# Optimization experiments

Measured on AMD Instinct MI355X. Metric: run time of the kernel, lower is better.

## Reference

```python
import jax, jax.numpy as jnp
import numpy as np

N = 4096
IN_DIM = 512
NUM_HEADS = 8
SUB_DIM = 64
ETA = 0.5
LAMBDA_SPARSE = 0.1
EDGE_PROB = 0.01


def setup_inputs() -> dict:
    key = jax.random.key(0)
    k_h, k_u, k_a = jax.random.split(key, 3)
    H = jax.random.normal(k_h, (N, IN_DIM), dtype=jnp.float32)
    # Per-head orthonormal subspace bases (QR init, as in the torch module)
    raw = jax.random.normal(k_u, (NUM_HEADS, IN_DIM, SUB_DIM), dtype=jnp.float32)
    U = jax.vmap(lambda a: jnp.linalg.qr(a)[0])(raw)  # [K, in_dim, r]
    # Binary adjacency mask with self-loops (float 0/1)
    adj = (jax.random.uniform(k_a, (N, N)) < EDGE_PROB).astype(jnp.float32)
    adj_mask = jnp.maximum(adj, jnp.eye(N, dtype=jnp.float32))
    threshold = jnp.full((IN_DIM,), LAMBDA_SPARSE, dtype=jnp.float32)
    return {"H": H, "adj_mask": adj_mask, "U": U, "threshold": threshold}


def reference(H, adj_mask, U, threshold):
    r = U.shape[-1]
    scale = jnp.asarray(r, H.dtype) ** 0.5
    # Z_k = U_k^T H^T  -> [K, r, n]
    Z = jnp.einsum('kdr,nd->krn', U, H)
    # scores[k, i, j] = Z_k[:, i] . Z_k[:, j] / sqrt(r), masked to neighbors
    scores = jnp.einsum('kri,krj->kij', Z, Z) / scale
    scores = scores + (1.0 - adj_mask) * (-1e9)
    alpha = jax.nn.softmax(scores, axis=-1)          # [K, n, n]
    # Z_agg[k, :, i] = sum_j alpha[k, i, j] * Z_k[:, j]
    Z_agg = jnp.einsum('krj,kij->kri', Z, alpha)      # [K, r, n]
    # project back and sum heads: [n, d]
    agg = jnp.einsum('kdr,kri->id', U, Z_agg)
    H_half = H + ETA * agg
    H_out = jax.nn.relu(H_half - threshold[None, :])
    # orthogonality loss: sum_{k<l} ||U_k^T U_l||_F^2
    gram = jnp.einsum('kdr,lds->klrs', U, U)
    sq = jnp.sum(gram ** 2, axis=(-1, -2))            # [K, K]
    orth_loss = 0.5 * (jnp.sum(sq) - jnp.trace(sq))
    return H_out, orth_loss
```

## Files before the change

### kernel.cpp

```cpp
#include <hip/hip_runtime.h>
#include <hip/hip_bf16.h>

#define NN   4096
#define DD   512
#define KH   8
#define RR   64
#define CAP  128

typedef unsigned short u16;
typedef unsigned int   u32;
typedef __attribute__((ext_vector_type(8))) short short8;
typedef __attribute__((ext_vector_type(4))) float f32x4;

__device__ __forceinline__ float bflo(u32 v){ union{u32 i; float f;} c; c.i = v << 16;        return c.f; }
__device__ __forceinline__ float bfhi(u32 v){ union{u32 i; float f;} c; c.i = v & 0xFFFF0000u; return c.f; }
__device__ __forceinline__ u16 f2bf(float f){ __hip_bfloat16 h = __float2bfloat16(f); return *reinterpret_cast<u16*>(&h); }

__global__ __launch_bounds__(256) void prep_all(const float* __restrict__ H, const float* __restrict__ U,
                                                u16* __restrict__ Hb, u16* __restrict__ Bt1,
                                                u16* __restrict__ Bt2, float* __restrict__ lossA,
                                                int* __restrict__ doneA) {
    __shared__ float tile[64][65];
    int b = blockIdx.x, t = threadIdx.x;
    if (b < 2048) {
        size_t id = (size_t)b * 256 + t;
        float4 v = *(const float4*)(H + id * 4);
        ushort4 o; o.x = f2bf(v.x); o.y = f2bf(v.y); o.z = f2bf(v.z); o.w = f2bf(v.w);
        *(ushort4*)(Hb + id * 4) = o;
        return;
    }
    if (b == 2112) { if (t == 0) { lossA[0] = 0.f; doneA[0] = 0; } return; }
    int b2 = b - 2048;
    int k = b2 >> 3, d0 = (b2 & 7) * 64;
    #pragma unroll
    for (int s = 0; s < 4; s++) {
        int u = t + 256 * s;
        int dd = u >> 4, rq = u & 15;
        float4 v = *(const float4*)(U + ((size_t)(k * DD + d0 + dd)) * RR + rq * 4);
        tile[dd][rq * 4 + 0] = v.x; tile[dd][rq * 4 + 1] = v.y;
        tile[dd][rq * 4 + 2] = v.z; tile[dd][rq * 4 + 3] = v.w;
    }
    __syncthreads();
    {
        int r = t >> 2;
        #pragma unroll
        for (int ii = 0; ii < 16; ii++) {
            int dd = (t & 3) * 16 + ii;
            Bt1[(size_t)(k * RR + r) * DD + d0 + dd] = f2bf(tile[dd][r]);
        }
    }
    {
        int dd = t >> 2, rb = (t & 3) * 16;
        #pragma unroll
        for (int ii = 0; ii < 16; ii++) {
            Bt2[(size_t)(d0 + dd) * DD + k * RR + rb + ii] = f2bf(tile[dd][rb + ii]);
        }
    }
}

__global__ __launch_bounds__(256) void zgemm_mfma(const u16* __restrict__ Hb, const u16* __restrict__ Bt1,
                                                  u16* __restrict__ Zb) {
    __shared__ short As[64][72];
    __shared__ short Bs[64][72];
    const int t = threadIdx.x;
    const int i0 = blockIdx.x * 64, n0 = blockIdx.y * 64;
    const int w = t >> 6, lane = t & 63;
    const int lm = lane & 15, lg = lane >> 4;
    f32x4 acc[4] = {};
    for (int kc = 0; kc < DD; kc += 64) {
        #pragma unroll
        for (int s = 0; s < 2; s++) {
            int c = t + 256 * s; int row = c >> 3, g = c & 7;
            *(short8*)&As[row][g * 8] = *(const short8*)(Hb  + (size_t)(i0 + row) * DD + kc + g * 8);
            *(short8*)&Bs[row][g * 8] = *(const short8*)(Bt1 + (size_t)(n0 + row) * DD + kc + g * 8);
        }
        __syncthreads();
        #pragma unroll
        for (int ks = 0; ks < 64; ks += 32) {
            short8 af = *(const short8*)&As[w * 16 + lm][ks + lg * 8];
            #pragma unroll
            for (int b = 0; b < 4; b++) {
                short8 bfr = *(const short8*)&Bs[b * 16 + lm][ks + lg * 8];
                acc[b] = __builtin_amdgcn_mfma_f32_16x16x32_bf16(af, bfr, acc[b], 0, 0, 0);
            }
        }
        __syncthreads();
    }
    #pragma unroll
    for (int b = 0; b < 4; b++)
        #pragma unroll
        for (int q = 0; q < 4; q++) {
            int row = i0 + w * 16 + lg * 4 + q;
            int col = n0 + b * 16 + lm;
            Zb[(size_t)row * DD + col] = f2bf(acc[b][q]);
        }
}

__global__ __launch_bounds__(512) void attn5(const u16* __restrict__ Zb, const float* __restrict__ adj,
                                             u16* __restrict__ Zaggb) {
    const int i = blockIdx.x, t = threadIdx.x;
    const int k = t >> 6, lane = t & 63;
    __shared__ int   nbrS[CAP + 32];
    __shared__ int   cntS;
    __shared__ float ziS[DD];
    __shared__ short zbuf[KH][32][72];
    if (t == 0) cntS = 0;
    __syncthreads();
    const float* arow = adj + (size_t)i * NN;
    #pragma unroll
    for (int qq = 0; qq < 2; qq++) {
        int j = (qq * 512 + t) * 4;
        float4 mv = *(const float4*)(arow + j);
        if (mv.x != 0.f) { int p = atomicAdd(&cntS, 1); if (p < CAP) nbrS[p] = j;     }
        if (mv.y != 0.f) { int p = atomicAdd(&cntS, 1); if (p < CAP) nbrS[p] = j + 1; }
        if (mv.z != 0.f) { int p = atomicAdd(&cntS, 1); if (p < CAP) nbrS[p] = j + 2; }
        if (mv.w != 0.f) { int p = atomicAdd(&cntS, 1); if (p < CAP) nbrS[p] = j + 3; }
    }
    if (t < 256) {
        u32 v = *(const u32*)(Zb + (size_t)i * DD + t * 2);
        ziS[t * 2] = bflo(v); ziS[t * 2 + 1] = bfhi(v);
    }
    __syncthreads();
    const int ci = min(cntS, CAP);
    if (t < 32) nbrS[ci + t] = nbrS[0];
    __syncthreads();

    const int n = lane >> 1, h = lane & 1;
    const int half = lane >> 5, L = lane & 31;
    const float4* zi4 = (const float4*)(ziS + k * 64 + h * 32);
    float m = -3.0e38f, l = 0.f, accA = 0.f, accB = 0.f;

    for (int base = 0; base < ci; base += 32) {
        const int cact = min(32, ci - base);
        const int j = nbrS[base + n];
        const uint4* zp = (const uint4*)(Zb + (size_t)j * DD + k * 64 + h * 32);
        uint4 v0 = zp[0], v1 = zp[1], v2 = zp[2], v3 = zp[3];
        *(uint4*)&zbuf[k][n][h * 32 + 0]  = v0;
        *(uint4*)&zbuf[k][n][h * 32 + 8]  = v1;
        *(uint4*)&zbuf[k][n][h * 32 + 16] = v2;
        *(uint4*)&zbuf[k][n][h * 32 + 24] = v3;
        float4 a0 = zi4[0], a1 = zi4[1], a2 = zi4[2], a3 = zi4[3];
        float4 a4 = zi4[4], a5 = zi4[5], a6 = zi4[6], a7 = zi4[7];
        float s = bflo(v0.x)*a0.x + bfhi(v0.x)*a0.y + bflo(v0.y)*a0.z + bfhi(v0.y)*a0.w
                + bflo(v0.z)*a1.x + bfhi(v0.z)*a1.y + bflo(v0.w)*a1.z + bfhi(v0.w)*a1.w
                + bflo(v1.x)*a2.x + bfhi(v1.x)*a2.y + bflo(v1.y)*a2.z + bfhi(v1.y)*a2.w
                + bflo(v1.z)*a3.x + bfhi(v1.z)*a3.y + bflo(v1.w)*a3.z + bfhi(v1.w)*a3.w
                + bflo(v2.x)*a4.x + bfhi(v2.x)*a4.y + bflo(v2.y)*a4.z + bfhi(v2.y)*a4.w
                + bflo(v2.z)*a5.x + bfhi(v2.z)*a5.y + bflo(v2.w)*a5.z + bfhi(v2.w)*a5.w
                + bflo(v3.x)*a6.x + bfhi(v3.x)*a6.y + bflo(v3.y)*a6.z + bfhi(v3.y)*a6.w
                + bflo(v3.z)*a7.x + bfhi(v3.z)*a7.y + bflo(v3.w)*a7.z + bfhi(v3.w)*a7.w;
        s += __shfl_xor(s, 1);
        s *= 0.125f;
        if (n >= cact) s = -3.0e38f;
        float mx = s;
        #pragma unroll
        for (int off = 2; off < 64; off <<= 1) mx = fmaxf(mx, __shfl_xor(mx, off));
        const float mnew = fmaxf(m, mx);
        const float scale = __expf(m - mnew);
        const float e = (n < cact) ? __expf(s - mnew) : 0.f;
        float se = h ? 0.f : e;
        #pragma unroll
        for (int off = 1; off < 64; off <<= 1) se += __shfl_xor(se, off);
        l = l * scale + se;
        m = mnew;
        accA *= scale; accB *= scale;
        for (int c = half; c < cact; c += 2) {
            const float wgt = __shfl(e, 2 * c);
            u32 z2 = *(const u32*)&zbuf[k][c][2 * L];
            accA += wgt * bflo(z2);
            accB += wgt * bfhi(z2);
        }
    }
    accA += __shfl_xor(accA, 32);
    accB += __shfl_xor(accB, 32);
    if (lane < 32) {
        const float inv = 1.0f / l;
        u32 o = ((u32)f2bf(accA * inv)) | (((u32)f2bf(accB * inv)) << 16);
        *(u32*)(Zaggb + (size_t)i * DD + k * 64 + 2 * L) = o;
    }
}

__global__ __launch_bounds__(256) void outgemm_mfma(const u16* __restrict__ Ab, const u16* __restrict__ Btb,
                                                    const float* __restrict__ H, const float* __restrict__ thr,
                                                    float* __restrict__ out) {
    __shared__ short As[64][72];
    __shared__ short Bs[64][72];
    const int t = threadIdx.x;
    const int i0 = blockIdx.x * 64, n0 = blockIdx.y * 64;
    const int w = t >> 6, lane = t & 63;
    const int lm = lane & 15, lg = lane >> 4;
    f32x4 acc[4] = {};
    for (int kc = 0; kc < DD; kc += 64) {
        #pragma unroll
        for (int s = 0; s < 2; s++) {
            int c = t + 256 * s; int row = c >> 3, g = c & 7;
            *(short8*)&As[row][g * 8] = *(const short8*)(Ab  + (size_t)(i0 + row) * DD + kc + g * 8);
            *(short8*)&Bs[row][g * 8] = *(const short8*)(Btb + (size_t)(n0 + row) * DD + kc + g * 8);
        }
        __syncthreads();
        #pragma unroll
        for (int ks = 0; ks < 64; ks += 32) {
            short8 af = *(const short8*)&As[w * 16 + lm][ks + lg * 8];
            #pragma unroll
            for (int b = 0; b < 4; b++) {
                short8 bfr = *(const short8*)&Bs[b * 16 + lm][ks + lg * 8];
                acc[b] = __builtin_amdgcn_mfma_f32_16x16x32_bf16(af, bfr, acc[b], 0, 0, 0);
            }
        }
        __syncthreads();
    }
    #pragma unroll
    for (int b = 0; b < 4; b++) {
        const int col = n0 + b * 16 + lm;
        const float th = thr[col];
        #pragma unroll
        for (int q = 0; q < 4; q++) {
            int row = i0 + w * 16 + lg * 4 + q;
            float h = H[(size_t)row * DD + col];
            out[(size_t)row * DD + col] = fmaxf(h + 0.5f * acc[b][q] - th, 0.f);
        }
    }
}

__global__ __launch_bounds__(256) void orth_kernel(const float* __restrict__ U, float* __restrict__ loss,
                                                   int* __restrict__ done, float* __restrict__ outLoss) {
    __shared__ float UkT[64][20];
    __shared__ float UlT[64][68];
    const int pb = blockIdx.x >> 2, strip = blockIdx.x & 3;
    int idx = pb, k = 0, lh = 1;
    #pragma unroll
    for (int kk = 0; kk < 8; kk++) {
        int c = 7 - kk;
        if (idx < c) { k = kk; lh = kk + 1 + idx; break; }
        idx -= c;
    }
    const int t = threadIdx.x;
    const int r = t & 15;
    const int s0 = (t >> 4) * 4;
    const int r0g = strip * 16;
    const float* Uk = U + (size_t)k  * DD * RR;
    const float* Ul = U + (size_t)lh * DD * RR;
    float a0 = 0.f, a1 = 0.f, a2 = 0.f, a3 = 0.f;
    for (int dc = 0; dc < DD; dc += 64) {
        {   int dd = t >> 2, rq = t & 3;
            *(float4*)&UkT[dd][rq * 4] = *(const float4*)(Uk + (size_t)(dc + dd) * RR + r0g + rq * 4);
        }
        #pragma unroll
        for (int s = 0; s < 4; s++) {
            int u = t + 256 * s;
            int dd = u >> 4, sq = u & 15;
            *(float4*)&UlT[dd][sq * 4] = *(const float4*)(Ul + (size_t)(dc + dd) * RR + sq * 4);
        }
        __syncthreads();
        #pragma unroll 4
        for (int dd = 0; dd < 64; dd++) {
            float a = UkT[dd][r];
            float4 b = *(const float4*)&UlT[dd][s0];
            a0 += a * b.x; a1 += a * b.y; a2 += a * b.z; a3 += a * b.w;
        }
        __syncthreads();
    }
    float v = a0 * a0 + a1 * a1 + a2 * a2 + a3 * a3;
    #pragma unroll
    for (int off = 32; off; off >>= 1) v += __shfl_down(v, off, 64);
    __shared__ float red[4];
    if ((t & 63) == 0) red[t >> 6] = v;
    __syncthreads();
    if (t == 0) {
        atomicAdd(loss, red[0] + red[1] + red[2] + red[3]);
        __threadfence();
        int d = atomicAdd(done, 1);
        if (d == 111) {
            float total = atomicAdd(loss, 0.f);
            outLoss[0] = total;
        }
    }
}

extern "C" void kernel_launch(void* const* d_in, const int* in_sizes, int n_in,
                              void* d_out, int out_size, void* d_ws, size_t ws_size,
                              hipStream_t stream) {
    const float* H   = (const float*)d_in[0];
    const float* adj = (const float*)d_in[1];
    const float* U   = (const float*)d_in[2];
    const float* thr = (const float*)d_in[3];
    float* out = (float*)d_out;

    char* ws = (char*)d_ws;
    float* lossA = (float*)ws;
    int*   doneA = (int*)(ws + 64);
    u16*   Hb    = (u16*)(ws + 1024);
    u16*   Zb    = (u16*)(ws + 1024 + 4u * 1024 * 1024);
    u16*   Zaggb = (u16*)(ws + 1024 + 8u * 1024 * 1024);
    u16*   Bt1   = (u16*)(ws + 1024 + 12u * 1024 * 1024);
    u16*   Bt2   = (u16*)(ws + 1024 + 12u * 1024 * 1024 + 512u * 1024);

    prep_all<<<2113, 256, 0, stream>>>(H, U, Hb, Bt1, Bt2, lossA, doneA);
    zgemm_mfma<<<dim3(64, 8), 256, 0, stream>>>(Hb, Bt1, Zb);
    attn5<<<NN, 512, 0, stream>>>(Zb, adj, Zaggb);
    outgemm_mfma<<<dim3(64, 8), 256, 0, stream>>>(Zaggb, Bt2, H, thr, out);
    orth_kernel<<<112, 256, 0, stream>>>(U, lossA, doneA, out + (size_t)NN * DD);
}
```

Before: 179.6 us.

## Fuse adjacency scan, Z GEMM and orth loss into one kernel; slim attention tiles

Result: slower. 197.5 us (+10.0%).

```diff
diff --git a/kernel.cpp b/kernel.cpp
--- a/kernel.cpp
+++ b/kernel.cpp
@@ -58,115 +58,177 @@
     }
 }
 
-__global__ __launch_bounds__(256) void zgemm_mfma(const u16* __restrict__ Hb, const u16* __restrict__ Bt1,
-                                                  u16* __restrict__ Zb) {
-    __shared__ short As[64][72];
-    __shared__ short Bs[64][72];
-    const int t = threadIdx.x;
-    const int i0 = blockIdx.x * 64, n0 = blockIdx.y * 64;
-    const int w = t >> 6, lane = t & 63;
-    const int lm = lane & 15, lg = lane >> 4;
-    f32x4 acc[4] = {};
-    for (int kc = 0; kc < DD; kc += 64) {
-        #pragma unroll
-        for (int s = 0; s < 2; s++) {
-            int c = t + 256 * s; int row = c >> 3, g = c & 7;
-            *(short8*)&As[row][g * 8] = *(const short8*)(Hb  + (size_t)(i0 + row) * DD + kc + g * 8);
-            *(short8*)&Bs[row][g * 8] = *(const short8*)(Bt1 + (size_t)(n0 + row) * DD + kc + g * 8);
-        }
-        __syncthreads();
-        #pragma unroll
-        for (int ks = 0; ks < 64; ks += 32) {
-            short8 af = *(const short8*)&As[w * 16 + lm][ks + lg * 8];
+struct GemmSh { short As[64][72]; short Bs[64][72]; };
+struct OrthSh { float UkT[64][20]; float UlT[64][68]; float red[4]; };
+struct ScanSh { int cnt; };
+union  MidSh  { GemmSh g; OrthSh o; ScanSh s; };
+
+__global__ __launch_bounds__(256) void mid_kernel(const u16* __restrict__ Hb, const u16* __restrict__ Bt1,
+                                                  u16* __restrict__ Zb,
+                                                  const float* __restrict__ adj, int* __restrict__ nlist,
+                                                  int* __restrict__ cnt,
+                                                  const float* __restrict__ U, float* __restrict__ loss,
+                                                  int* __restrict__ done, float* __restrict__ outLoss) {
+    __shared__ MidSh sh;
+    const int b = blockIdx.x, t = threadIdx.x;
+    if (b < 4096) {
+        const int i = b;
+        if (t == 0) sh.s.cnt = 0;
+        __syncthreads();
+        const float* arow = adj + (size_t)i * NN;
+        #pragma unroll
+        for (int qq = 0; qq < 4; qq++) {
+            int j = (qq * 256 + t) * 4;
+            float4 mv = *(const float4*)(arow + j);
+            if (mv.x != 0.f) { int p = atomicAdd(&sh.s.cnt, 1); if (p < CAP) nlist[(size_t)i * CAP + p] = j;     }
+            if (mv.y != 0.f) { int p = atomicAdd(&sh.s.cnt, 1); if (p < CAP) nlist[(size_t)i * CAP + p] = j + 1; }
+            if (mv.z != 0.f) { int p = atomicAdd(&sh.s.cnt, 1); if (p < CAP) nlist[(size_t)i * CAP + p] = j + 2; }
+            if (mv.w != 0.f) { int p = atomicAdd(&sh.s.cnt, 1); if (p < CAP) nlist[(size_t)i * CAP + p] = j + 3; }
+        }
+        __syncthreads();
+        if (t == 0) cnt[i] = min(sh.s.cnt, CAP);
+        return;
+    }
+    if (b < 4608) {
+        const int bb = b - 4096;
+        const int i0 = (bb & 63) * 64, n0 = (bb >> 6) * 64;
+        const int w = t >> 6, lane = t & 63;
+        const int lm = lane & 15, lg = lane >> 4;
+        f32x4 acc[4] = {};
+        for (int kc = 0; kc < DD; kc += 64) {
             #pragma unroll
-            for (int b = 0; b < 4; b++) {
-                short8 bfr = *(const short8*)&Bs[b * 16 + lm][ks + lg * 8];
-                acc[b] = __builtin_amdgcn_mfma_f32_16x16x32_bf16(af, bfr, acc[b], 0, 0, 0);
+            for (int s = 0; s < 2; s++) {
+                int c = t + 256 * s; int row = c >> 3, g = c & 7;
+                *(short8*)&sh.g.As[row][g * 8] = *(const short8*)(Hb  + (size_t)(i0 + row) * DD + kc + g * 8);
+                *(short8*)&sh.g.Bs[row][g * 8] = *(const short8*)(Bt1 + (size_t)(n0 + row) * DD + kc + g * 8);
             }
-        }
-        __syncthreads();
-    }
+            __syncthreads();
+            #pragma unroll
+            for (int ks = 0; ks < 64; ks += 32) {
+                short8 af = *(const short8*)&sh.g.As[w * 16 + lm][ks + lg * 8];
+                #pragma unroll
+                for (int bq = 0; bq < 4; bq++) {
+                    short8 bfr = *(const short8*)&sh.g.Bs[bq * 16 + lm][ks + lg * 8];
+                    acc[bq] = __builtin_amdgcn_mfma_f32_16x16x32_bf16(af, bfr, acc[bq], 0, 0, 0);
+                }
+            }
+            __syncthreads();
+        }
+        #pragma unroll
+        for (int bq = 0; bq < 4; bq++)
+            #pragma unroll
+            for (int q = 0; q < 4; q++) {
+                int row = i0 + w * 16 + lg * 4 + q;
+                int col = n0 + bq * 16 + lm;
+                Zb[(size_t)row * DD + col] = f2bf(acc[bq][q]);
+            }
+        return;
+    }
+    const int ob = b - 4608;
+    const int pb = ob >> 2, strip = ob & 3;
+    int idx = pb, k = 0, lh = 1;
     #pragma unroll
-    for (int b = 0; b < 4; b++)
-        #pragma unroll
-        for (int q = 0; q < 4; q++) {
-            int row = i0 + w * 16 + lg * 4 + q;
-            int col = n0 + b * 16 + lm;
-            Zb[(size_t)row * DD + col] = f2bf(acc[b][q]);
-        }
-}
-
-__global__ __launch_bounds__(512) void attn5(const u16* __restrict__ Zb, const float* __restrict__ adj,
-                                             u16* __restrict__ Zaggb) {
+    for (int kk = 0; kk < 8; kk++) {
+        int c = 7 - kk;
+        if (idx < c) { k = kk; lh = kk + 1 + idx; break; }
+        idx -= c;
+    }
+    const int r = t & 15;
+    const int s0 = (t >> 4) * 4;
+    const int r0g = strip * 16;
+    const float* Uk = U + (size_t)k  * DD * RR;
+    const float* Ul = U + (size_t)lh * DD * RR;
+    float a0 = 0.f, a1 = 0.f, a2 = 0.f, a3 = 0.f;
+    for (int dc = 0; dc < DD; dc += 64) {
+        {   int dd = t >> 2, rq = t & 3;
+            *(float4*)&sh.o.UkT[dd][rq * 4] = *(const float4*)(Uk + (size_t)(dc + dd) * RR + r0g + rq * 4);
+        }
+        #pragma unroll
+        for (int s = 0; s < 4; s++) {
+            int u = t + 256 * s;
+            int dd = u >> 4, sq = u & 15;
+            *(float4*)&sh.o.UlT[dd][sq * 4] = *(const float4*)(Ul + (size_t)(dc + dd) * RR + sq * 4);
+        }
+        __syncthreads();
+        #pragma unroll 4
+        for (int dd = 0; dd < 64; dd++) {
+            float a = sh.o.UkT[dd][r];
+            float4 bv = *(const float4*)&sh.o.UlT[dd][s0];
+            a0 += a * bv.x; a1 += a * bv.y; a2 += a * bv.z; a3 += a * bv.w;
+        }
+        __syncthreads();
+    }
+    float v = a0 * a0 + a1 * a1 + a2 * a2 + a3 * a3;
+    #pragma unroll
+    for (int off = 32; off; off >>= 1) v += __shfl_down(v, off, 64);
+    if ((t & 63) == 0) sh.o.red[t >> 6] = v;
+    __syncthreads();
+    if (t == 0) {
+        atomicAdd(loss, sh.o.red[0] + sh.o.red[1] + sh.o.red[2] + sh.o.red[3]);
+        __threadfence();
+        int d = atomicAdd(done, 1);
+        if (d == 111) {
+            float total = atomicAdd(loss, 0.f);
+            outLoss[0] = total;
+        }
+    }
+}
+
+__global__ __launch_bounds__(512) void attn6(const u16* __restrict__ Zb, const int* __restrict__ nlist,
+                                             const int* __restrict__ cnt, u16* __restrict__ Zaggb) {
     const int i = blockIdx.x, t = threadIdx.x;
     const int k = t >> 6, lane = t & 63;
-    __shared__ int   nbrS[CAP + 32];
-    __shared__ int   cntS;
+    __shared__ int   nbrS[CAP + 16];
     __shared__ float ziS[DD];
-    __shared__ short zbuf[KH][32][72];
-    if (t == 0) cntS = 0;
-    __syncthreads();
-    const float* arow = adj + (size_t)i * NN;
-    #pragma unroll
-    for (int qq = 0; qq < 2; qq++) {
-        int j = (qq * 512 + t) * 4;
-        float4 mv = *(const float4*)(arow + j);
-        if (mv.x != 0.f) { int p = atomicAdd(&cntS, 1); if (p < CAP) nbrS[p] = j;     }
-        if (mv.y != 0.f) { int p = atomicAdd(&cntS, 1); if (p < CAP) nbrS[p] = j + 1; }
-        if (mv.z != 0.f) { int p = atomicAdd(&cntS, 1); if (p < CAP) nbrS[p] = j + 2; }
-        if (mv.w != 0.f) { int p = atomicAdd(&cntS, 1); if (p < CAP) nbrS[p] = j + 3; }
-    }
+    __shared__ u32   zbufU[KH][16][36];
+    const int ci = cnt[i];
+    for (int u = t; u < ci; u += 512) nbrS[u] = nlist[(size_t)i * CAP + u];
     if (t < 256) {
         u32 v = *(const u32*)(Zb + (size_t)i * DD + t * 2);
         ziS[t * 2] = bflo(v); ziS[t * 2 + 1] = bfhi(v);
     }
     __syncthreads();
-    const int ci = min(cntS, CAP);
-    if (t < 32) nbrS[ci + t] = nbrS[0];
+    if (t < 16) nbrS[ci + t] = nbrS[0];
     __syncthreads();
 
-    const int n = lane >> 1, h = lane & 1;
+    const int n = lane >> 2, q = lane & 3;
     const int half = lane >> 5, L = lane & 31;
-    const float4* zi4 = (const float4*)(ziS + k * 64 + h * 32);
+    const float4* zi4 = (const float4*)(ziS + k * 64 + q * 16);
     float m = -3.0e38f, l = 0.f, accA = 0.f, accB = 0.f;
 
-    for (int base = 0; base < ci; base += 32) {
-        const int cact = min(32, ci - base);
+    for (int base = 0; base < ci; base += 16) {
+        const int cact = min(16, ci - base);
         const int j = nbrS[base + n];
-        const uint4* zp = (const uint4*)(Zb + (size_t)j * DD + k * 64 + h * 32);
-        uint4 v0 = zp[0], v1 = zp[1], v2 = zp[2], v3 = zp[3];
-        *(uint4*)&zbuf[k][n][h * 32 + 0]  = v0;
-        *(uint4*)&zbuf[k][n][h * 32 + 8]  = v1;
-        *(uint4*)&zbuf[k][n][h * 32 + 16] = v2;
-        *(uint4*)&zbuf[k][n][h * 32 + 24] = v3;
+        __builtin_amdgcn_wave_barrier();
+        const uint4* zp = (const uint4*)(Zb + (size_t)j * DD + k * 64 + q * 16);
+        uint4 v0 = zp[0], v1 = zp[1];
+        *(uint4*)&zbufU[k][n][q * 8]     = v0;
+        *(uint4*)&zbufU[k][n][q * 8 + 4] = v1;
         float4 a0 = zi4[0], a1 = zi4[1], a2 = zi4[2], a3 = zi4[3];
-        float4 a4 = zi4[4], a5 = zi4[5], a6 = zi4[6], a7 = zi4[7];
         float s = bflo(v0.x)*a0.x + bfhi(v0.x)*a0.y + bflo(v0.y)*a0.z + bfhi(v0.y)*a0.w
                 + bflo(v0.z)*a1.x + bfhi(v0.z)*a1.y + bflo(v0.w)*a1.z + bfhi(v0.w)*a1.w
                 + bflo(v1.x)*a2.x + bfhi(v1.x)*a2.y + bflo(v1.y)*a2.z + bfhi(v1.y)*a2.w
-                + bflo(v1.z)*a3.x + bfhi(v1.z)*a3.y + bflo(v1.w)*a3.z + bfhi(v1.w)*a3.w
-                + bflo(v2.x)*a4.x + bfhi(v2.x)*a4.y + bflo(v2.y)*a4.z + bfhi(v2.y)*a4.w
-                + bflo(v2.z)*a5.x + bfhi(v2.z)*a5.y + bflo(v2.w)*a5.z + bfhi(v2.w)*a5.w
-                + bflo(v3.x)*a6.x + bfhi(v3.x)*a6.y + bflo(v3.y)*a6.z + bfhi(v3.y)*a6.w
-                + bflo(v3.z)*a7.x + bfhi(v3.z)*a7.y + bflo(v3.w)*a7.z + bfhi(v3.w)*a7.w;
+                + bflo(v1.z)*a3.x + bfhi(v1.z)*a3.y + bflo(v1.w)*a3.z + bfhi(v1.w)*a3.w;
         s += __shfl_xor(s, 1);
+        s += __shfl_xor(s, 2);
         s *= 0.125f;
         if (n >= cact) s = -3.0e38f;
         float mx = s;
         #pragma unroll
-        for (int off = 2; off < 64; off <<= 1) mx = fmaxf(mx, __shfl_xor(mx, off));
+        for (int off = 4; off < 64; off <<= 1) mx = fmaxf(mx, __shfl_xor(mx, off));
         const float mnew = fmaxf(m, mx);
         const float scale = __expf(m - mnew);
         const float e = (n < cact) ? __expf(s - mnew) : 0.f;
-        float se = h ? 0.f : e;
-        #pragma unroll
-        for (int off = 1; off < 64; off <<= 1) se += __shfl_xor(se, off);
+        float se = e;
+        #pragma unroll
+        for (int off = 4; off < 64; off <<= 1) se += __shfl_xor(se, off);
         l = l * scale + se;
         m = mnew;
         accA *= scale; accB *= scale;
+        __builtin_amdgcn_wave_barrier();
         for (int c = half; c < cact; c += 2) {
-            const float wgt = __shfl(e, 2 * c);
-            u32 z2 = *(const u32*)&zbuf[k][c][2 * L];
+            const float wgt = __shfl(e, 4 * c);
+            u32 z2 = zbufU[k][c][L];
             accA += wgt * bflo(z2);
             accB += wgt * bfhi(z2);
         }
@@ -222,61 +284,6 @@
     }
 }
 
-__global__ __launch_bounds__(256) void orth_kernel(const float* __restrict__ U, float* __restrict__ loss,
-                                                   int* __restrict__ done, float* __restrict__ outLoss) {
-    __shared__ float UkT[64][20];
-    __shared__ float UlT[64][68];
-    const int pb = blockIdx.x >> 2, strip = blockIdx.x & 3;
-    int idx = pb, k = 0, lh = 1;
-    #pragma unroll
-    for (int kk = 0; kk < 8; kk++) {
-        int c = 7 - kk;
-        if (idx < c) { k = kk; lh = kk + 1 + idx; break; }
-        idx -= c;
-    }
-    const int t = threadIdx.x;
-    const int r = t & 15;
-    const int s0 = (t >> 4) * 4;
-    const int r0g = strip * 16;
-    const float* Uk = U + (size_t)k  * DD * RR;
-    const float* Ul = U + (size_t)lh * DD * RR;
-    float a0 = 0.f, a1 = 0.f, a2 = 0.f, a3 = 0.f;
-    for (int dc = 0; dc < DD; dc += 64) {
-        {   int dd = t >> 2, rq = t & 3;
-            *(float4*)&UkT[dd][rq * 4] = *(const float4*)(Uk + (size_t)(dc + dd) * RR + r0g + rq * 4);
-        }
-        #pragma unroll
-        for (int s = 0; s < 4; s++) {
-            int u = t + 256 * s;
-            int dd = u >> 4, sq = u & 15;
-            *(float4*)&UlT[dd][sq * 4] = *(const float4*)(Ul + (size_t)(dc + dd) * RR + sq * 4);
-        }
-        __syncthreads();
-        #pragma unroll 4
-        for (int dd = 0; dd < 64; dd++) {
-            float a = UkT[dd][r];
-            float4 b = *(const float4*)&UlT[dd][s0];
-            a0 += a * b.x; a1 += a * b.y; a2 += a * b.z; a3 += a * b.w;
-        }
-        __syncthreads();
-    }
-    float v = a0 * a0 + a1 * a1 + a2 * a2 + a3 * a3;
-    #pragma unroll
-    for (int off = 32; off; off >>= 1) v += __shfl_down(v, off, 64);
-    __shared__ float red[4];
-    if ((t & 63) == 0) red[t >> 6] = v;
-    __syncthreads();
-    if (t == 0) {
-        atomicAdd(loss, red[0] + red[1] + red[2] + red[3]);
-        __threadfence();
-        int d = atomicAdd(done, 1);
-        if (d == 111) {
-            float total = atomicAdd(loss, 0.f);
-            outLoss[0] = total;
-        }
-    }
-}
-
 extern "C" void kernel_launch(void* const* d_in, const int* in_sizes, int n_in,
                               void* d_out, int out_size, void* d_ws, size_t ws_size,
                               hipStream_t stream) {
@@ -294,10 +301,12 @@
     u16*   Zaggb = (u16*)(ws + 1024 + 8u * 1024 * 1024);
     u16*   Bt1   = (u16*)(ws + 1024 + 12u * 1024 * 1024);
     u16*   Bt2   = (u16*)(ws + 1024 + 12u * 1024 * 1024 + 512u * 1024);
+    int*   nlist = (int*)(ws + 1024 + 13u * 1024 * 1024);
+    int*   cnt   = (int*)(ws + 1024 + 15u * 1024 * 1024 + 512u * 1024);
 
     prep_all<<<2113, 256, 0, stream>>>(H, U, Hb, Bt1, Bt2, lossA, doneA);
-    zgemm_mfma<<<dim3(64, 8), 256, 0, stream>>>(Hb, Bt1, Zb);
-    attn5<<<NN, 512, 0, stream>>>(Zb, adj, Zaggb);
+    mid_kernel<<<4720, 256, 0, stream>>>(Hb, Bt1, Zb, adj, nlist, cnt,
+                                         U, lossA, doneA, out + (size_t)NN * DD);
+    attn6<<<NN, 512, 0, stream>>>(Zb, nlist, cnt, Zaggb);
     outgemm_mfma<<<dim3(64, 8), 256, 0, stream>>>(Zaggb, Bt2, H, thr, out);
-    orth_kernel<<<112, 256, 0, stream>>>(U, lossA, doneA, out + (size_t)NN * DD);
-}
+}
```

## Move adjacency scan into prep kernel and shrink attention chunk to 16 neighbors

Applied to the files above, without the earlier changes.

Result: faster. 173.6 us (-3.4%).

```diff
diff --git a/kernel.cpp b/kernel.cpp
--- a/kernel.cpp
+++ b/kernel.cpp
@@ -16,22 +16,46 @@
 __device__ __forceinline__ float bfhi(u32 v){ union{u32 i; float f;} c; c.i = v & 0xFFFF0000u; return c.f; }
 __device__ __forceinline__ u16 f2bf(float f){ __hip_bfloat16 h = __float2bfloat16(f); return *reinterpret_cast<u16*>(&h); }
 
-__global__ __launch_bounds__(256) void prep_all(const float* __restrict__ H, const float* __restrict__ U,
-                                                u16* __restrict__ Hb, u16* __restrict__ Bt1,
-                                                u16* __restrict__ Bt2, float* __restrict__ lossA,
-                                                int* __restrict__ doneA) {
+__global__ __launch_bounds__(256) void prep_scan(const float* __restrict__ H, const float* __restrict__ U,
+                                                 const float* __restrict__ adj,
+                                                 u16* __restrict__ Hb, u16* __restrict__ Bt1,
+                                                 u16* __restrict__ Bt2,
+                                                 int* __restrict__ nlist, int* __restrict__ cnt,
+                                                 float* __restrict__ lossA, int* __restrict__ doneA) {
     __shared__ float tile[64][65];
-    int b = blockIdx.x, t = threadIdx.x;
-    if (b < 2048) {
-        size_t id = (size_t)b * 256 + t;
+    __shared__ int   list[CAP];
+    __shared__ int   cntS;
+    const int b = blockIdx.x, t = threadIdx.x;
+    if (b < 4096) {
+        const int i = b;
+        if (t == 0) cntS = 0;
+        __syncthreads();
+        const float* arow = adj + (size_t)i * NN;
+        #pragma unroll
+        for (int qq = 0; qq < 4; qq++) {
+            int j = (qq * 256 + t) * 4;
+            float4 mv = *(const float4*)(arow + j);
+            if (mv.x != 0.f) { int p = atomicAdd(&cntS, 1); if (p < CAP) list[p] = j;     }
+            if (mv.y != 0.f) { int p = atomicAdd(&cntS, 1); if (p < CAP) list[p] = j + 1; }
+            if (mv.z != 0.f) { int p = atomicAdd(&cntS, 1); if (p < CAP) list[p] = j + 2; }
+            if (mv.w != 0.f) { int p = atomicAdd(&cntS, 1); if (p < CAP) list[p] = j + 3; }
+        }
+        __syncthreads();
+        const int n = min(cntS, CAP);
+        if (t < n) nlist[(size_t)i * CAP + t] = list[t];
+        if (t == 0) cnt[i] = n;
+        return;
+    }
+    if (b < 6144) {
+        size_t id = (size_t)(b - 4096) * 256 + t;
         float4 v = *(const float4*)(H + id * 4);
         ushort4 o; o.x = f2bf(v.x); o.y = f2bf(v.y); o.z = f2bf(v.z); o.w = f2bf(v.w);
         *(ushort4*)(Hb + id * 4) = o;
         return;
     }
-    if (b == 2112) { if (t == 0) { lossA[0] = 0.f; doneA[0] = 0; } return; }
-    int b2 = b - 2048;
-    int k = b2 >> 3, d0 = (b2 & 7) * 64;
+    if (b == 6208) { if (t == 0) { lossA[0] = 0.f; doneA[0] = 0; } return; }
+    const int b2 = b - 6144;
+    const int k = b2 >> 3, d0 = (b2 & 7) * 64;
     #pragma unroll
     for (int s = 0; s < 4; s++) {
         int u = t + 256 * s;
@@ -41,16 +65,14 @@
         tile[dd][rq * 4 + 2] = v.z; tile[dd][rq * 4 + 3] = v.w;
     }
     __syncthreads();
-    {
-        int r = t >> 2;
+    {   int r = t >> 2;
         #pragma unroll
         for (int ii = 0; ii < 16; ii++) {
             int dd = (t & 3) * 16 + ii;
             Bt1[(size_t)(k * RR + r) * DD + d0 + dd] = f2bf(tile[dd][r]);
         }
     }
-    {
-        int dd = t >> 2, rb = (t & 3) * 16;
+    {   int dd = t >> 2, rb = (t & 3) * 16;
         #pragma unroll
         for (int ii = 0; ii < 16; ii++) {
             Bt2[(size_t)(d0 + dd) * DD + k * RR + rb + ii] = f2bf(tile[dd][rb + ii]);
@@ -96,80 +118,66 @@
         }
 }
 
-__global__ __launch_bounds__(512) void attn5(const u16* __restrict__ Zb, const float* __restrict__ adj,
-                                             u16* __restrict__ Zaggb) {
+__global__ __launch_bounds__(512) void attn7(const u16* __restrict__ Zb, const int* __restrict__ nlist,
+                                             const int* __restrict__ cnt, u16* __restrict__ Zaggb) {
     const int i = blockIdx.x, t = threadIdx.x;
     const int k = t >> 6, lane = t & 63;
-    __shared__ int   nbrS[CAP + 32];
-    __shared__ int   cntS;
+    __shared__ int   nbrS[CAP + 16];
     __shared__ float ziS[DD];
-    __shared__ short zbuf[KH][32][72];
-    if (t == 0) cntS = 0;
-    __syncthreads();
-    const float* arow = adj + (size_t)i * NN;
-    #pragma unroll
-    for (int qq = 0; qq < 2; qq++) {
-        int j = (qq * 512 + t) * 4;
-        float4 mv = *(const float4*)(arow + j);
-        if (mv.x != 0.f) { int p = atomicAdd(&cntS, 1); if (p < CAP) nbrS[p] = j;     }
-        if (mv.y != 0.f) { int p = atomicAdd(&cntS, 1); if (p < CAP) nbrS[p] = j + 1; }
-        if (mv.z != 0.f) { int p = atomicAdd(&cntS, 1); if (p < CAP) nbrS[p] = j + 2; }
-        if (mv.w != 0.f) { int p = atomicAdd(&cntS, 1); if (p < CAP) nbrS[p] = j + 3; }
-    }
+    __shared__ u32   zbufU[KH][16][36];
+    __shared__ float wS[KH][16];
+    const int ci = cnt[i];
+    for (int u = t; u < ci; u += 512) nbrS[u] = nlist[(size_t)i * CAP + u];
     if (t < 256) {
         u32 v = *(const u32*)(Zb + (size_t)i * DD + t * 2);
         ziS[t * 2] = bflo(v); ziS[t * 2 + 1] = bfhi(v);
     }
     __syncthreads();
-    const int ci = min(cntS, CAP);
-    if (t < 32) nbrS[ci + t] = nbrS[0];
+    if (t < 16) nbrS[ci + t] = nbrS[0];
     __syncthreads();
 
-    const int n = lane >> 1, h = lane & 1;
+    const int n = lane >> 2, q = lane & 3;
     const int half = lane >> 5, L = lane & 31;
-    const float4* zi4 = (const float4*)(ziS + k * 64 + h * 32);
+    const float4* zi4 = (const float4*)(ziS + k * 64 + q * 16);
     float m = -3.0e38f, l = 0.f, accA = 0.f, accB = 0.f;
 
-    for (int base = 0; base < ci; base += 32) {
-        const int cact = min(32, ci - base);
+    for (int base = 0; base < ci; base += 16) {
+        const int cact = min(16, ci - base);
         const int j = nbrS[base + n];
-        const uint4* zp = (const uint4*)(Zb + (size_t)j * DD + k * 64 + h * 32);
-        uint4 v0 = zp[0], v1 = zp[1], v2 = zp[2], v3 = zp[3];
-        *(uint4*)&zbuf[k][n][h * 32 + 0]  = v0;
-        *(uint4*)&zbuf[k][n][h * 32 + 8]  = v1;
-        *(uint4*)&zbuf[k][n][h * 32 + 16] = v2;
-        *(uint4*)&zbuf[k][n][h * 32 + 24] = v3;
+        const uint4* zp = (const uint4*)(Zb + (size_t)j * DD + k * 64 + q * 16);
+        uint4 v0 = zp[0], v1 = zp[1];
+        *(uint4*)&zbufU[k][n][q * 8]     = v0;
+        *(uint4*)&zbufU[k][n][q * 8 + 4] = v1;
         float4 a0 = zi4[0], a1 = zi4[1], a2 = zi4[2], a3 = zi4[3];
-        float4 a4 = zi4[4], a5 = zi4[5], a6 = zi4[6], a7 = zi4[7];
         float s = bflo(v0.x)*a0.x + bfhi(v0.x)*a0.y + bflo(v0.y)*a0.z + bfhi(v0.y)*a0.w
                 + bflo(v0.z)*a1.x + bfhi(v0.z)*a1.y + bflo(v0.w)*a1.z + bfhi(v0.w)*a1.w
                 + bflo(v1.x)*a2.x + bfhi(v1.x)*a2.y + bflo(v1.y)*a2.z + bfhi(v1.y)*a2.w
-                + bflo(v1.z)*a3.x + bfhi(v1.z)*a3.y + bflo(v1.w)*a3.z + bfhi(v1.w)*a3.w
-                + bflo(v2.x)*a4.x + bfhi(v2.x)*a4.y + bflo(v2.y)*a4.z + bfhi(v2.y)*a4.w
-                + bflo(v2.z)*a5.x + bfhi(v2.z)*a5.y + bflo(v2.w)*a5.z + bfhi(v2.w)*a5.w
-                + bflo(v3.x)*a6.x + bfhi(v3.x)*a6.y + bflo(v3.y)*a6.z + bfhi(v3.y)*a6.w
-                + bflo(v3.z)*a7.x + bfhi(v3.z)*a7.y + bflo(v3.w)*a7.z + bfhi(v3.w)*a7.w;
+                + bflo(v1.z)*a3.x + bfhi(v1.z)*a3.y + bflo(v1.w)*a3.z + bfhi(v1.w)*a3.w;
         s += __shfl_xor(s, 1);
+        s += __shfl_xor(s, 2);
         s *= 0.125f;
         if (n >= cact) s = -3.0e38f;
         float mx = s;
         #pragma unroll
-        for (int off = 2; off < 64; off <<= 1) mx = fmaxf(mx, __shfl_xor(mx, off));
+        for (int off = 4; off < 64; off <<= 1) mx = fmaxf(mx, __shfl_xor(mx, off));
         const float mnew = fmaxf(m, mx);
         const float scale = __expf(m - mnew);
         const float e = (n < cact) ? __expf(s - mnew) : 0.f;
-        float se = h ? 0.f : e;
-        #pragma unroll
-        for (int off = 1; off < 64; off <<= 1) se += __shfl_xor(se, off);
+        float se = e;
+        #pragma unroll
+        for (int off = 4; off < 64; off <<= 1) se += __shfl_xor(se, off);
         l = l * scale + se;
         m = mnew;
         accA *= scale; accB *= scale;
+        if (q == 0) wS[k][n] = e;
+        __syncthreads();
         for (int c = half; c < cact; c += 2) {
-            const float wgt = __shfl(e, 2 * c);
-            u32 z2 = *(const u32*)&zbuf[k][c][2 * L];
+            const float wgt = wS[k][c];
+            u32 z2 = zbufU[k][c][L];
             accA += wgt * bflo(z2);
             accB += wgt * bfhi(z2);
         }
+        __syncthreads();
     }
     accA += __shfl_xor(accA, 32);
     accB += __shfl_xor(accB, 32);
@@ -255,8 +263,8 @@
         #pragma unroll 4
         for (int dd = 0; dd < 64; dd++) {
             float a = UkT[dd][r];
-            float4 b = *(const float4*)&UlT[dd][s0];
-            a0 += a * b.x; a1 += a * b.y; a2 += a * b.z; a3 += a * b.w;
+            float4 bv = *(const float4*)&UlT[dd][s0];
+            a0 += a * bv.x; a1 += a * bv.y; a2 += a * bv.z; a3 += a * bv.w;
         }
         __syncthreads();
     }
@@ -294,10 +302,12 @@
     u16*   Zaggb = (u16*)(ws + 1024 + 8u * 1024 * 1024);
     u16*   Bt1   = (u16*)(ws + 1024 + 12u * 1024 * 1024);
     u16*   Bt2   = (u16*)(ws + 1024 + 12u * 1024 * 1024 + 512u * 1024);
-
-    prep_all<<<2113, 256, 0, stream>>>(H, U, Hb, Bt1, Bt2, lossA, doneA);
+    int*   nlist = (int*)(ws + 1024 + 13u * 1024 * 1024);
+    int*   cnt   = (int*)(ws + 1024 + 15u * 1024 * 1024 + 512u * 1024);
+
+    prep_scan<<<6209, 256, 0, stream>>>(H, U, adj, Hb, Bt1, Bt2, nlist, cnt, lossA, doneA);
     zgemm_mfma<<<dim3(64, 8), 256, 0, stream>>>(Hb, Bt1, Zb);
-    attn5<<<NN, 512, 0, stream>>>(Zb, adj, Zaggb);
+    attn7<<<NN, 512, 0, stream>>>(Zb, nlist, cnt, Zaggb);
     outgemm_mfma<<<dim3(64, 8), 256, 0, stream>>>(Zaggb, Bt2, H, thr, out);
     orth_kernel<<<112, 256, 0, stream>>>(U, lossA, doneA, out + (size_t)NN * DD);
 }
```
